# Kernel optimization log

Measured on AMD Instinct MI355X. Metric: run time of the kernel, lower is better.

The kernel has to match this reference:

```python
import jax, jax.numpy as jnp
import numpy as np

N = 100000   # nodes
E = 1600000  # edges
F_IN = 128
H = 128
C = 20


def setup_inputs() -> dict:
    key = jax.random.key(0)
    ks = jax.random.split(key, 12)
    s = lambda k, sh: jax.random.normal(k, sh, dtype=jnp.float32) * 0.05
    return {
        "x": jax.random.normal(ks[0], (N, F_IN), dtype=jnp.float32),
        "edge_index": jax.random.randint(ks[1], (2, E), 0, N, dtype=jnp.int64),
        # SAGEConv1: lin_l (neighbor, with bias), lin_r (root, no bias)
        "W1l": s(ks[2], (H, F_IN)), "b1": jnp.zeros((H,), jnp.float32), "W1r": s(ks[3], (H, F_IN)),
        # SAGEConv2
        "W2l": s(ks[4], (H, H)), "b2": jnp.zeros((H,), jnp.float32), "W2r": s(ks[5], (H, H)),
        # MLP head
        "Wm1": s(ks[6], (H, H)), "bm1": jnp.zeros((H,), jnp.float32),
        "Wm2": s(ks[7], (C, H)), "bm2": jnp.zeros((C,), jnp.float32),
    }


def _sage_conv(x, src, dst, Wl, bl, Wr):
    # PyG SAGEConv (aggr='mean'): out = lin_l(mean_{j in N(i)} x_j) + lin_r(x_i)
    msg = x[src]                                             # [E, d] irregular gather
    agg = jax.ops.segment_sum(msg, dst, num_segments=N)      # [N, d] scatter-add
    cnt = jax.ops.segment_sum(jnp.ones((msg.shape[0], 1), x.dtype), dst, num_segments=N)
    mean = agg / jnp.maximum(cnt, 1.0)
    return mean @ Wl.T + bl + x @ Wr.T


def reference(x, edge_index, W1l, b1, W1r, W2l, b2, W2r, Wm1, bm1, Wm2, bm2):
    src, dst = edge_index[0], edge_index[1]
    # two SAGEConv layers, each followed by relu (dropout = identity at eval)
    h = jax.nn.relu(_sage_conv(x, src, dst, W1l, b1, W1r))
    h = jax.nn.relu(_sage_conv(h, src, dst, W2l, b2, W2r))
    # MLP: Linear -> dropout(identity) -> ReLU -> Linear, then sigmoid
    h = jax.nn.relu(h @ Wm1.T + bm1)
    return jax.nn.sigmoid(h @ Wm2.T + bm2)
```

## Files before the change

kernel.cpp:

```cpp
#include <hip/hip_runtime.h>
#include <math.h>

#define NODES 100000
#define EDGES 1600000
#define HF 128
#define NC 20
#define CAPN 64
#define BSHIFT 8
#define BNODES 256
#define NBK ((NODES + BNODES - 1) / BNODES)
#define CAP 4608
#define EPB 4096
#define NPB ((EDGES + EPB - 1) / EPB)
#define XB ((NODES * HF / 8 + 255) / 256)

typedef __attribute__((ext_vector_type(8))) short bf16x8;
typedef __attribute__((ext_vector_type(4))) float f32x4;
typedef __attribute__((ext_vector_type(2))) float f32x2;

__device__ __forceinline__ ushort f2b(float f) {
    uint u = __float_as_uint(f);
    uint r = (u + 0x7FFFu + ((u >> 16) & 1u)) >> 16;
    return (ushort)r;
}
__device__ __forceinline__ uchar f2q(float f) {
    return (uchar)(__builtin_amdgcn_cvt_pk_fp8_f32(f, f, 0, false) & 0xFF);
}

__global__ void prep_kernel(const float* __restrict__ x, ushort* __restrict__ xb,
                            uchar* __restrict__ xq,
                            const float* __restrict__ a, const float* __restrict__ b,
                            const float* __restrict__ c, const float* __restrict__ d,
                            const float* __restrict__ e, const float* __restrict__ wm2,
                            ushort* __restrict__ wb,
                            const int* __restrict__ src, const int* __restrict__ dst,
                            int* __restrict__ bcur, uint2* __restrict__ ebuf,
                            int n8, int E) {
    __shared__ int h[NBK];
    __shared__ int basea[NBK];
    int blk = blockIdx.x;
    int t = threadIdx.x;
    if (blk < NPB) {
        int base = blk * EPB;
        for (int i = t; i < NBK; i += 256) h[i] = 0;
        __syncthreads();
        for (int i = t; i < EPB; i += 256) {
            int ee = base + i;
            if (ee < E) atomicAdd(&h[dst[ee] >> BSHIFT], 1);
        }
        __syncthreads();
        for (int i = t; i < NBK; i += 256) {
            int cc = h[i];
            basea[i] = cc ? (i * CAP + atomicAdd(&bcur[i], cc)) : 0;
        }
        __syncthreads();
        for (int i = t; i < NBK; i += 256) h[i] = 0;
        __syncthreads();
        for (int i = t; i < EPB; i += 256) {
            int ee = base + i;
            if (ee < E) {
                int dd = dst[ee];
                int bb = dd >> BSHIFT;
                int pos = basea[bb] + atomicAdd(&h[bb], 1);
                ebuf[pos] = make_uint2((uint)src[ee], (uint)dd);
            }
        }
    } else if (blk < NPB + XB) {
        int i = (blk - NPB) * 256 + t;
        if (i >= n8) return;
        const float4* p = (const float4*)x + (size_t)i * 2;
        float4 va = p[0], vb = p[1];
        uint4 o;
        o.x = (uint)f2b(va.x) | ((uint)f2b(va.y) << 16);
        o.y = (uint)f2b(va.z) | ((uint)f2b(va.w) << 16);
        o.z = (uint)f2b(vb.x) | ((uint)f2b(vb.y) << 16);
        o.w = (uint)f2b(vb.z) | ((uint)f2b(vb.w) << 16);
        ((uint4*)xb)[i] = o;
        uint2 q;
        q.x = __builtin_amdgcn_cvt_pk_fp8_f32(va.x, va.y, 0, false);
        q.x = __builtin_amdgcn_cvt_pk_fp8_f32(va.z, va.w, q.x, true);
        q.y = __builtin_amdgcn_cvt_pk_fp8_f32(vb.x, vb.y, 0, false);
        q.y = __builtin_amdgcn_cvt_pk_fp8_f32(vb.z, vb.w, q.y, true);
        ((uint2*)xq)[i] = q;
    } else {
        int i = (blk - NPB - XB) * 256 + t;
        if (i < 81920) {
            const float* srcs[5] = {a, b, c, d, e};
            wb[i] = f2b(srcs[i >> 14][i & 16383]);
        } else if (i < 86016) {
            int j = i - 81920;
            wb[i] = ((j >> 7) < NC) ? f2b(wm2[j]) : (ushort)0;
        }
    }
}

__global__ void csr_build(const uint2* __restrict__ ebuf, const int* __restrict__ bcur,
                          int* __restrict__ cnt, int* __restrict__ ssrcp) {
    int b = blockIdx.x;
    int t = threadIdx.x;
    int e0 = b * CAP;
    int cnt_b = bcur[b];
    for (int i = t; i < cnt_b; i += 256) {
        uint2 ed = ebuf[e0 + i];
        int slot = atomicAdd(&cnt[ed.y], 1);
        if (slot < CAPN)
            ssrcp[(size_t)ed.y * CAPN + slot] = (int)ed.x;
    }
}

template<bool EMITQ, bool FUSE>
__global__ __launch_bounds__(512)
void fused_sage_layer(const uchar* __restrict__ Xq, const ushort* __restrict__ X,
                      const int* __restrict__ ssrcp, const int* __restrict__ cnt,
                      const ushort* __restrict__ Wl, const ushort* __restrict__ Wr,
                      const float* __restrict__ bias, ushort* __restrict__ out,
                      uchar* __restrict__ outq,
                      const ushort* __restrict__ Wm1b, const ushort* __restrict__ Wm2b,
                      const float* __restrict__ bm1, const float* __restrict__ bm2,
                      float* __restrict__ fout, int n) {
    __shared__ ushort sh[64][136];
    __shared__ int sidx[64 * CAPN];
    __shared__ int s_len[64];
    int row0b = blockIdx.x * 64;
    int t = threadIdx.x;

    if (t < 64) {
        int node = row0b + t;
        s_len[t] = (node < n) ? min(cnt[node], CAPN) : 0;
    }
    int nrows = min(64, n - row0b);
    int lim = nrows * CAPN;
    const int* wsrc = ssrcp + (size_t)row0b * CAPN;
    for (int i = t; i < lim; i += 512) sidx[i] = wsrc[i] << 7;
    __syncthreads();

    {
        int sub = t & 31;
        int sel = sub >> 3;
        int cg = sub & 7;
        const uchar* xc = Xq + cg * 16;
        for (int batch = 0; batch < 4; ++batch) {
            int nloc = batch * 16 + (t >> 5);
            int node = row0b + nloc;
            f32x2 acc2[8];
#pragma unroll
            for (int i = 0; i < 8; ++i) acc2[i] = f32x2{0.f, 0.f};
            int len = s_len[nloc];
            int sbase = nloc * CAPN;

            for (int e = 0; e < len; e += 16) {
                uint4 v[4];
#pragma unroll
                for (int w = 0; w < 4; ++w) {
                    int ee = e + 4 * w + sel;
                    int off = sidx[sbase + ee];
                    uint4 vv = {0u, 0u, 0u, 0u};
                    if (ee < len)
                        vv = *(const uint4*)(xc + (size_t)(uint)off);
                    v[w] = vv;
                }
#pragma unroll
                for (int w = 0; w < 4; ++w) {
                    const uint* pp = (const uint*)&v[w];
#pragma unroll
                    for (int i = 0; i < 4; ++i) {
                        f32x2 lof = __builtin_amdgcn_cvt_pk_f32_fp8(pp[i], false);
                        f32x2 hif = __builtin_amdgcn_cvt_pk_f32_fp8(pp[i], true);
                        acc2[2 * i]     += lof;
                        acc2[2 * i + 1] += hif;
                    }
                }
            }
#pragma unroll
            for (int i = 0; i < 8; ++i) {
                acc2[i].x += __shfl_xor(acc2[i].x, 8);
                acc2[i].x += __shfl_xor(acc2[i].x, 16);
                acc2[i].y += __shfl_xor(acc2[i].y, 8);
                acc2[i].y += __shfl_xor(acc2[i].y, 16);
            }
            if (sel == 0 && node < n) {
                float invd = 1.0f / fmaxf((float)len, 1.0f);
                uint4 o0, o1;
                uint* p0 = (uint*)&o0;
                uint* p1 = (uint*)&o1;
#pragma unroll
                for (int i = 0; i < 4; ++i) {
                    p0[i] = (uint)f2b(acc2[i].x * invd) | ((uint)f2b(acc2[i].y * invd) << 16);
                    p1[i] = (uint)f2b(acc2[4 + i].x * invd) | ((uint)f2b(acc2[4 + i].y * invd) << 16);
                }
                *(uint4*)(&sh[nloc][cg * 16]) = o0;
                *(uint4*)(&sh[nloc][cg * 16 + 8]) = o1;
            }
        }
    }
    __syncthreads();

    int wave = t >> 6;
    int lane = t & 63;
    int m = lane & 15, quad = lane >> 4;
    int col = wave * 16 + m;

    bf16x8 bl[4], br[4];
#pragma unroll
    for (int ks = 0; ks < 4; ++ks) {
        bl[ks] = *(const bf16x8*)(Wl + (size_t)col * HF + ks * 32 + quad * 8);
        br[ks] = *(const bf16x8*)(Wr + (size_t)col * HF + ks * 32 + quad * 8);
    }
    float bia = bias[col];

    if (!FUSE) {
#pragma unroll
        for (int rt = 0; rt < 4; ++rt) {
            int row0 = row0b + rt * 16;
            if (row0 >= n) break;
            f32x4 acc = {0.f, 0.f, 0.f, 0.f};
            const ushort* arow = X + (size_t)(row0 + m) * HF + quad * 8;
#pragma unroll
            for (int ks = 0; ks < 4; ++ks) {
                bf16x8 a = *(const bf16x8*)(&sh[rt * 16 + m][ks * 32 + quad * 8]);
                acc = __builtin_amdgcn_mfma_f32_16x16x32_bf16(a, bl[ks], acc, 0, 0, 0);
                bf16x8 ar = *(const bf16x8*)(arow + ks * 32);
                acc = __builtin_amdgcn_mfma_f32_16x16x32_bf16(ar, br[ks], acc, 0, 0, 0);
            }
#pragma unroll
            for (int i = 0; i < 4; ++i) {
                int r = row0 + quad * 4 + i;
                if (r < n) {
                    float v = fmaxf(acc[i] + bia, 0.f);
                    out[(size_t)r * HF + col] = f2b(v);
                    if (EMITQ) outq[(size_t)r * HF + col] = f2q(v);
                }
            }
        }
    } else {
        f32x4 accs[4];
#pragma unroll
        for (int rt = 0; rt < 4; ++rt) {
            int row0 = row0b + rt * 16;
            f32x4 acc = {0.f, 0.f, 0.f, 0.f};
            if (row0 < n) {
                const ushort* arow = X + (size_t)(row0 + m) * HF + quad * 8;
#pragma unroll
                for (int ks = 0; ks < 4; ++ks) {
                    bf16x8 a = *(const bf16x8*)(&sh[rt * 16 + m][ks * 32 + quad * 8]);
                    acc = __builtin_amdgcn_mfma_f32_16x16x32_bf16(a, bl[ks], acc, 0, 0, 0);
                    bf16x8 ar = *(const bf16x8*)(arow + ks * 32);
                    acc = __builtin_amdgcn_mfma_f32_16x16x32_bf16(ar, br[ks], acc, 0, 0, 0);
                }
            }
            accs[rt] = acc;
        }
        __syncthreads();
#pragma unroll
        for (int rt = 0; rt < 4; ++rt)
#pragma unroll
            for (int i = 0; i < 4; ++i)
                sh[rt * 16 + quad * 4 + i][col] = f2b(fmaxf(accs[rt][i] + bia, 0.f));
        __syncthreads();

        bf16x8 w1[4];
#pragma unroll
        for (int ks = 0; ks < 4; ++ks)
            w1[ks] = *(const bf16x8*)(Wm1b + (size_t)col * HF + ks * 32 + quad * 8);
        float hb = bm1[col];
        f32x4 hacc[4];
#pragma unroll
        for (int rt = 0; rt < 4; ++rt) {
            f32x4 acc = {0.f, 0.f, 0.f, 0.f};
#pragma unroll
            for (int ks = 0; ks < 4; ++ks) {
                bf16x8 a = *(const bf16x8*)(&sh[rt * 16 + m][ks * 32 + quad * 8]);
                acc = __builtin_amdgcn_mfma_f32_16x16x32_bf16(a, w1[ks], acc, 0, 0, 0);
            }
            hacc[rt] = acc;
        }
        __syncthreads();
#pragma unroll
        for (int rt = 0; rt < 4; ++rt)
#pragma unroll
            for (int i = 0; i < 4; ++i)
                sh[rt * 16 + quad * 4 + i][col] = f2b(fmaxf(hacc[rt][i] + hb, 0.f));
        __syncthreads();

        if (wave < 4) {
            bf16x8 c0f[4], c1f[4];
#pragma unroll
            for (int ks = 0; ks < 4; ++ks) {
                c0f[ks] = *(const bf16x8*)(Wm2b + (size_t)m * HF + ks * 32 + quad * 8);
                c1f[ks] = *(const bf16x8*)(Wm2b + (size_t)(16 + m) * HF + ks * 32 + quad * 8);
            }
            f32x4 o0 = {0.f, 0.f, 0.f, 0.f};
            f32x4 o1 = {0.f, 0.f, 0.f, 0.f};
#pragma unroll
            for (int ks = 0; ks < 4; ++ks) {
                bf16x8 a = *(const bf16x8*)(&sh[wave * 16 + m][ks * 32 + quad * 8]);
                o0 = __builtin_amdgcn_mfma_f32_16x16x32_bf16(a, c0f[ks], o0, 0, 0, 0);
                o1 = __builtin_amdgcn_mfma_f32_16x16x32_bf16(a, c1f[ks], o1, 0, 0, 0);
            }
            float bb0 = bm2[m];
            float bb1 = (m < 4) ? bm2[16 + m] : 0.f;
#pragma unroll
            for (int i = 0; i < 4; ++i) {
                int row = row0b + wave * 16 + quad * 4 + i;
                if (row < n) {
                    fout[(size_t)row * NC + m] = 1.0f / (1.0f + expf(-(o0[i] + bb0)));
                    if (m < 4)
                        fout[(size_t)row * NC + 16 + m] = 1.0f / (1.0f + expf(-(o1[i] + bb1)));
                }
            }
        }
    }
}

extern "C" void kernel_launch(void* const* d_in, const int* in_sizes, int n_in,
                              void* d_out, int out_size, void* d_ws, size_t ws_size,
                              hipStream_t stream) {
    const float* x   = (const float*)d_in[0];
    const int*   ei  = (const int*)d_in[1];
    const float* W1l = (const float*)d_in[2];
    const float* b1  = (const float*)d_in[3];
    const float* W1r = (const float*)d_in[4];
    const float* W2l = (const float*)d_in[5];
    const float* b2  = (const float*)d_in[6];
    const float* W2r = (const float*)d_in[7];
    const float* Wm1 = (const float*)d_in[8];
    const float* bm1 = (const float*)d_in[9];
    const float* Wm2 = (const float*)d_in[10];
    const float* bm2 = (const float*)d_in[11];
    float* out = (float*)d_out;

    const int N = NODES, E = EDGES;
    const int* src = ei;
    const int* dst = ei + E;

    int* cnt    = (int*)d_ws;
    int* bcur   = cnt + 100352;
    int* ssrcp  = bcur + 512;
    ushort* xb  = (ushort*)(ssrcp + (size_t)N * CAPN);
    ushort* h1  = xb + (size_t)N * HF;
    uint2* ebuf = (uint2*)h1;
    ushort* wb  = h1 + (size_t)N * HF;
    uchar* xq   = (uchar*)(wb + 86016);
    uchar* h1q  = xq + (size_t)N * HF;
    ushort* wb1l = wb;
    ushort* wb1r = wb + 16384;
    ushort* wb2l = wb + 32768;
    ushort* wb2r = wb + 49152;
    ushort* wbm1 = wb + 65536;
    ushort* wbm2 = wb + 81920;

    const int n8 = N * HF / 8;

    hipMemsetAsync(cnt, 0, (100352 + 512) * sizeof(int), stream);
    prep_kernel<<<NPB + XB + 336, 256, 0, stream>>>(
        x, xb, xq, W1l, W1r, W2l, W2r, Wm1, Wm2, wb, src, dst, bcur, ebuf, n8, E);
    csr_build<<<NBK, 256, 0, stream>>>(ebuf, bcur, cnt, ssrcp);

    const int fusedBlocks = (N + 63) / 64;

    fused_sage_layer<true, false><<<fusedBlocks, 512, 0, stream>>>(
        xq, xb, ssrcp, cnt, wb1l, wb1r, b1, h1, h1q,
        nullptr, nullptr, nullptr, nullptr, nullptr, N);
    fused_sage_layer<false, true><<<fusedBlocks, 512, 0, stream>>>(
        h1q, h1, ssrcp, cnt, wb2l, wb2r, b2, nullptr, nullptr,
        wbm1, wbm2, bm1, bm2, out, N);
}
```

Measured before the change: 330.6 us.

## Use LDS-local counters in CSR build and prefetch next node's neighbor gather

csr_build now counts slots in a shared-memory array per 256-node bucket instead of using global atomics, then writes the per-node counts out once. This removes global atomic traffic and shrinks the memset to only the bucket cursors. The aggregation loop in the fused SAGE layer software-pipelines the first 16-neighbor gather of the next node batch while accumulating the current one, to hide gather latency. This costs extra registers, which may lower occupancy.

```diff
diff --git a/kernel.cpp b/kernel.cpp
--- a/kernel.cpp
+++ b/kernel.cpp
@@ -96,16 +96,24 @@
 
 __global__ void csr_build(const uint2* __restrict__ ebuf, const int* __restrict__ bcur,
                           int* __restrict__ cnt, int* __restrict__ ssrcp) {
+    __shared__ int lcnt[BNODES];
     int b = blockIdx.x;
     int t = threadIdx.x;
+    lcnt[t] = 0;
+    __syncthreads();
     int e0 = b * CAP;
-    int cnt_b = bcur[b];
-    for (int i = t; i < cnt_b; i += 256) {
+    int cb = bcur[b];
+    int nbase = b << BSHIFT;
+    for (int i = t; i < cb; i += 256) {
         uint2 ed = ebuf[e0 + i];
-        int slot = atomicAdd(&cnt[ed.y], 1);
+        int loc = ed.y & (BNODES - 1);
+        int slot = atomicAdd(&lcnt[loc], 1);
         if (slot < CAPN)
-            ssrcp[(size_t)ed.y * CAPN + slot] = (int)ed.x;
-    }
+            ssrcp[(size_t)(nbase + loc) * CAPN + slot] = (int)ed.x;
+    }
+    __syncthreads();
+    int node = nbase + t;
+    if (node < NODES) cnt[node] = lcnt[t];
 }
 
 template<bool EMITQ, bool FUSE>
@@ -135,28 +143,61 @@
     __syncthreads();
 
     {
+        int grp = t >> 5;
         int sub = t & 31;
         int sel = sub >> 3;
         int cg = sub & 7;
         const uchar* xc = Xq + cg * 16;
+
+        uint4 vA[4], vB[4];
+        int lenN = s_len[grp];
+#pragma unroll
+        for (int w = 0; w < 4; ++w) {
+            int ee = 4 * w + sel;
+            int off = sidx[grp * CAPN + ee];
+            uint4 vv = {0u, 0u, 0u, 0u};
+            if (ee < lenN) vv = *(const uint4*)(xc + (size_t)(uint)off);
+            vA[w] = vv;
+        }
+#pragma unroll
         for (int batch = 0; batch < 4; ++batch) {
-            int nloc = batch * 16 + (t >> 5);
+            int nloc = batch * 16 + grp;
             int node = row0b + nloc;
+            int len = lenN;
+            int sbase = nloc * CAPN;
+            if (batch < 3) {
+                int nn = (batch + 1) * 16 + grp;
+                lenN = s_len[nn];
+                int sb = nn * CAPN;
+#pragma unroll
+                for (int w = 0; w < 4; ++w) {
+                    int ee = 4 * w + sel;
+                    int off = sidx[sb + ee];
+                    uint4 vv = {0u, 0u, 0u, 0u};
+                    if (ee < lenN) vv = *(const uint4*)(xc + (size_t)(uint)off);
+                    vB[w] = vv;
+                }
+            }
             f32x2 acc2[8];
 #pragma unroll
             for (int i = 0; i < 8; ++i) acc2[i] = f32x2{0.f, 0.f};
-            int len = s_len[nloc];
-            int sbase = nloc * CAPN;
-
-            for (int e = 0; e < len; e += 16) {
+#pragma unroll
+            for (int w = 0; w < 4; ++w) {
+                const uint* pp = (const uint*)&vA[w];
+#pragma unroll
+                for (int i = 0; i < 4; ++i) {
+                    acc2[2 * i]     += __builtin_amdgcn_cvt_pk_f32_fp8(pp[i], false);
+                    acc2[2 * i + 1] += __builtin_amdgcn_cvt_pk_f32_fp8(pp[i], true);
+                }
+            }
+            for (int e = 16; e < len; e += 16) {
                 uint4 v[4];
 #pragma unroll
                 for (int w = 0; w < 4; ++w) {
                     int ee = e + 4 * w + sel;
                     int off = sidx[sbase + ee];
                     uint4 vv = {0u, 0u, 0u, 0u};
-                    if (ee < len)
-                        vv = *(const uint4*)(xc + (size_t)(uint)off);
+                    if (ee < len) vv = *(const uint4*)(xc + (size_t)(uint)off);
                     v[w] = vv;
                 }
 #pragma unroll
@@ -164,10 +205,8 @@
                     const uint* pp = (const uint*)&v[w];
 #pragma unroll
                     for (int i = 0; i < 4; ++i) {
-                        f32x2 lof = __builtin_amdgcn_cvt_pk_f32_fp8(pp[i], false);
-                        f32x2 hif = __builtin_amdgcn_cvt_pk_f32_fp8(pp[i], true);
-                        acc2[2 * i]     += lof;
-                        acc2[2 * i + 1] += hif;
+                        acc2[2 * i]     += __builtin_amdgcn_cvt_pk_f32_fp8(pp[i], false);
+                        acc2[2 * i + 1] += __builtin_amdgcn_cvt_pk_f32_fp8(pp[i], true);
                     }
                 }
             }
@@ -191,6 +230,8 @@
                 *(uint4*)(&sh[nloc][cg * 16]) = o0;
                 *(uint4*)(&sh[nloc][cg * 16 + 8]) = o1;
             }
+#pragma unroll
+            for (int w = 0; w < 4; ++w) vA[w] = vB[w];
         }
     }
     __syncthreads();
@@ -351,7 +392,7 @@
 
     const int n8 = N * HF / 8;
 
-    hipMemsetAsync(cnt, 0, (100352 + 512) * sizeof(int), stream);
+    hipMemsetAsync(bcur, 0, 512 * sizeof(int), stream);
     prep_kernel<<<NPB + XB + 336, 256, 0, stream>>>(
         x, xb, xq, W1l, W1r, W2l, W2r, Wm1, Wm2, wb, src, dst, bcur, ebuf, n8, E);
     csr_build<<<NBK, 256, 0, stream>>>(ebuf, bcur, cnt, ssrcp);
```

After: 305.8 us. -7.5%, faster.
